# Kernel optimization log

Measured on AMD Instinct MI355X. Metric: run time of the kernel, lower is better.

The kernel has to match this reference:

```python
import jax, jax.numpy as jnp
import numpy as np
import math

B, S, D, H = 2, 2048, 1024, 16
DK = D // H

def setup_inputs() -> dict:
    key = jax.random.key(0)
    ks = jax.random.split(key, 12)
    scale = 0.02
    return {
        "q": jax.random.normal(ks[0], (B, S, D), jnp.float32),
        "k": jax.random.normal(ks[1], (B, S, D), jnp.float32),
        "v": jax.random.normal(ks[2], (B, S, D), jnp.float32),
        "mask": jnp.ones((B, S), jnp.int32),
        "Wq": jax.random.normal(ks[3], (D, D), jnp.float32) * scale,
        "bq": jnp.zeros((D,), jnp.float32),
        "Wk": jax.random.normal(ks[4], (D, D), jnp.float32) * scale,
        "bk": jnp.zeros((D,), jnp.float32),
        "Wv": jax.random.normal(ks[5], (D, D), jnp.float32) * scale,
        "bv": jnp.zeros((D,), jnp.float32),
        "Wo": jax.random.normal(ks[6], (D, D), jnp.float32) * scale,
        "bo": jnp.zeros((D,), jnp.float32),
    }

def _split_heads(x):
    b, s, d = x.shape
    return x.reshape(b, s, H, DK).transpose(0, 2, 1, 3)  # [b,h,s,dk]

def reference(q, k, v, mask, Wq, bq, Wk, bk, Wv, bv, Wo, bo):
    Q = _split_heads(q @ Wq.T + bq)
    K = _split_heads(k @ Wk.T + bk)
    V = _split_heads(v @ Wv.T + bv)
    scores = jnp.einsum('bhqd,bhkd->bhqk', Q, K) / math.sqrt(DK)
    # mask dim==2 path: [b,s] -> [b,1,1,s]
    m = mask[:, None, None, :]
    scores = jnp.where(m == 0, jnp.float32(-1e9), scores)
    attn = jax.nn.softmax(scores, axis=-1)  # dropout is identity in eval
    out = jnp.einsum('bhqk,bhkd->bhqd', attn, V)
    out = out.transpose(0, 2, 1, 3).reshape(q.shape[0], q.shape[1], D)
    return out @ Wo.T + bo
```

## Files before the change

### kernel.cpp

```cpp
#include <hip/hip_runtime.h>
#include <math.h>

#define D_MODEL 1024
#define NHEAD   16
#define DKH     64
#define SEQ     2048
#define BATCH   2
#define TOK     (BATCH*SEQ)

typedef short s16x8 __attribute__((ext_vector_type(8)));
typedef float f32x4 __attribute__((ext_vector_type(4)));
typedef float f32x16 __attribute__((ext_vector_type(16)));
typedef unsigned short ushort_t;

__device__ inline unsigned short f2bf(float f) {
    union { float f; unsigned u; } v; v.f = f;
    unsigned r = v.u + 0x7FFFu + ((v.u >> 16) & 1u);
    return (unsigned short)(r >> 16);
}
__device__ inline float bf2f(ushort_t h) {
    union { unsigned u; float f; } v; v.u = (unsigned)h << 16;
    return v.f;
}
__device__ inline unsigned cvt_pk_bf16(float a, float b) {
    unsigned r;
    asm("v_cvt_pk_bf16_f32 %0, %1, %2" : "=v"(r) : "v"(a), "v"(b));
    return r;
}
__device__ inline void gload16(const void* g, void* l) {
    __builtin_amdgcn_global_load_lds(
        (const __attribute__((address_space(1))) void*)g,
        (__attribute__((address_space(3))) void*)l, 16, 0, 0);
}
__device__ inline f32x16 zero16() {
    f32x16 v;
#pragma unroll
    for (int i = 0; i < 16; ++i) v[i] = 0.f;
    return v;
}

__global__ __launch_bounds__(256) void convert_all(
    const float* __restrict__ q, const float* __restrict__ k,
    const float* __restrict__ v,
    const float* __restrict__ Wq, const float* __restrict__ Wk,
    const float* __restrict__ Wv, const float* __restrict__ Wo,
    const int* __restrict__ mask,
    ushort_t* __restrict__ qb, ushort_t* __restrict__ kb,
    ushort_t* __restrict__ vb,
    ushort_t* __restrict__ Wqb, ushort_t* __restrict__ Wkb,
    ushort_t* __restrict__ Wvb, ushort_t* __restrict__ Wohi,
    ushort_t* __restrict__ Wolo, float* __restrict__ mb)
{
    const int ACT4 = TOK * D_MODEL / 4;
    const int W4   = D_MODEL * D_MODEL / 4;
    const int total = 3 * ACT4 + 4 * W4 + TOK / 4;
    for (int u = blockIdx.x * 256 + threadIdx.x; u < total; u += gridDim.x * 256) {
        if (u < 3 * ACT4) {
            int which = u / ACT4, off = u - which * ACT4;
            const float* src = which == 0 ? q : which == 1 ? k : v;
            ushort_t*    dst = which == 0 ? qb : which == 1 ? kb : vb;
            float4 f = ((const float4*)src)[off];
            uint2 o;
            o.x = cvt_pk_bf16(f.x, f.y);
            o.y = cvt_pk_bf16(f.z, f.w);
            ((uint2*)dst)[off] = o;
        } else if (u < 3 * ACT4 + 3 * W4) {
            int uu = u - 3 * ACT4;
            int which = uu / W4, off = uu - which * W4;
            const float* src = which == 0 ? Wq : which == 1 ? Wk : Wv;
            ushort_t*    dst = which == 0 ? Wqb : which == 1 ? Wkb : Wvb;
            float4 f = ((const float4*)src)[off];
            uint2 o;
            o.x = cvt_pk_bf16(f.x, f.y);
            o.y = cvt_pk_bf16(f.z, f.w);
            ((uint2*)dst)[off] = o;
        } else if (u < 3 * ACT4 + 4 * W4) {
            int off = u - (3 * ACT4 + 3 * W4);
            float4 f = ((const float4*)Wo)[off];
            ushort_t h0 = f2bf(f.x), h1 = f2bf(f.y), h2 = f2bf(f.z), h3 = f2bf(f.w);
            uint2 hw;
            hw.x = (unsigned)h0 | ((unsigned)h1 << 16);
            hw.y = (unsigned)h2 | ((unsigned)h3 << 16);
            ((uint2*)Wohi)[off] = hw;
            uint2 lw;
            lw.x = cvt_pk_bf16(f.x - bf2f(h0), f.y - bf2f(h1));
            lw.y = cvt_pk_bf16(f.z - bf2f(h2), f.w - bf2f(h3));
            ((uint2*)Wolo)[off] = lw;
        } else {
            int off = u - (3 * ACT4 + 4 * W4);
            int4 m = ((const int4*)mask)[off];
            float4 f;
            f.x = m.x ? 0.f : -1e9f;
            f.y = m.y ? 0.f : -1e9f;
            f.z = m.z ? 0.f : -1e9f;
            f.w = m.w ? 0.f : -1e9f;
            ((float4*)mb)[off] = f;
        }
    }
}

__global__ __launch_bounds__(256) void gemm_qkv(
    const ushort_t* __restrict__ qb, const ushort_t* __restrict__ kb,
    const ushort_t* __restrict__ vb,
    const ushort_t* __restrict__ Wqb, const ushort_t* __restrict__ Wkb,
    const ushort_t* __restrict__ Wvb,
    const float* __restrict__ bqp, const float* __restrict__ bkp,
    const float* __restrict__ bvp,
    ushort_t* __restrict__ Qb, ushort_t* __restrict__ Kb,
    ushort_t* __restrict__ Vtb)
{
    __shared__ __align__(16) char pool[64 * 136 * 2];
    ushort_t* As = (ushort_t*)pool;
    ushort_t* Ws = As + 128 * 32;

    const int z = blockIdx.z;
    const ushort_t* Ain  = z == 0 ? qb : z == 1 ? kb : vb;
    const ushort_t* Wptr = z == 0 ? Wqb : z == 1 ? Wkb : Wvb;
    const float*    bias = z == 0 ? bqp : z == 1 ? bkp : bvp;

    const int hwid = blockIdx.x + 8 * blockIdx.y;
    const int work = (hwid & 7) * 32 + (hwid >> 3);
    const int m0 = (work >> 3) * 128;
    const int n0 = (work & 7) * 128;

    const int t = threadIdx.x;
    const int w = t >> 6, lane = t & 63, l15 = lane & 15, l4 = lane >> 4;
    const int wr = w >> 1, wc = w & 1;

    f32x4 acc[4][4];
#pragma unroll
    for (int m = 0; m < 4; ++m)
#pragma unroll
        for (int n = 0; n < 4; ++n) acc[m][n] = (f32x4){0.f, 0.f, 0.f, 0.f};

    const int schunk = (t & 3) ^ ((t >> 2) & 3);
    const ushort_t* Ag = Ain  + (size_t)(m0 + (t >> 2)) * D_MODEL + schunk * 8;
    const ushort_t* Wg = Wptr + (size_t)(n0 + (t >> 2)) * D_MODEL + schunk * 8;
    ushort_t* AsW = As + w * 512;
    ushort_t* WsW = Ws + w * 512;
    const int fx = (l4 ^ (l15 & 3)) * 8;

    for (int k0 = 0; k0 < D_MODEL; k0 += 32) {
        __syncthreads();
        gload16(Ag + k0, AsW);
        gload16(Ag + (size_t)64 * D_MODEL + k0, AsW + 2048);
        gload16(Wg + k0, WsW);
        gload16(Wg + (size_t)64 * D_MODEL + k0, WsW + 2048);
        __syncthreads();

        s16x8 af[4], bfr[4];
#pragma unroll
        for (int m = 0; m < 4; ++m)
            af[m] = *(const s16x8*)&As[(wr * 64 + m * 16 + l15) * 32 + fx];
#pragma unroll
        for (int n = 0; n < 4; ++n)
            bfr[n] = *(const s16x8*)&Ws[(wc * 64 + n * 16 + l15) * 32 + fx];
#pragma unroll
        for (int m = 0; m < 4; ++m)
#pragma unroll
            for (int n = 0; n < 4; ++n)
                acc[m][n] = __builtin_amdgcn_mfma_f32_16x16x32_bf16(af[m], bfr[n], acc[m][n], 0, 0, 0);
    }

    if (z == 2) {
        ushort_t* Ct = (ushort_t*)pool;
        const int h0 = n0 >> 6;
        const int bb = m0 >> 11;
        const int s0 = m0 & (SEQ - 1);
#pragma unroll
        for (int hh = 0; hh < 2; ++hh) {
            __syncthreads();
            if (wc == hh) {
#pragma unroll
                for (int n = 0; n < 4; ++n) {
                    const int nl = n * 16 + l15;
                    const float bv = bias[n0 + hh * 64 + nl];
#pragma unroll
                    for (int m = 0; m < 4; ++m) {
                        const int ml = wr * 64 + m * 16 + l4 * 4;
#pragma unroll
                        for (int r = 0; r < 4; ++r)
                            Ct[nl * 136 + ml + r] = f2bf(acc[m][n][r] + bv);
                    }
                }
            }
            __syncthreads();
            const int dl = t >> 2;
            ushort_t* dst = Vtb + (((size_t)bb * NHEAD + h0 + hh) * DKH + dl) * SEQ + s0;
#pragma unroll
            for (int c = 0; c < 4; ++c) {
                int chk = (t & 3) + c * 4;
                *(uint4*)&dst[chk * 8] = *(const uint4*)&Ct[dl * 136 + chk * 8];
            }
        }
    } else {
        ushort_t* Cout = z == 0 ? Qb : Kb;
#pragma unroll
        for (int n = 0; n < 4; ++n) {
            const int col = n0 + wc * 64 + n * 16 + l15;
            const float bv = bias[col];
#pragma unroll
            for (int m = 0; m < 4; ++m) {
                const int row = m0 + wr * 64 + m * 16 + l4 * 4;
#pragma unroll
                for (int r = 0; r < 4; ++r)
                    Cout[(size_t)(row + r) * D_MODEL + col] = f2bf(acc[m][n][r] + bv);
            }
        }
    }
}

__global__ __launch_bounds__(256) void gemm_out(
    const ushort_t* __restrict__ Ain, const ushort_t* __restrict__ Wptr,
    const ushort_t* __restrict__ W2ptr, const float* __restrict__ bias,
    float* __restrict__ Cout)
{
    __shared__ ushort_t As[128 * 32];
    __shared__ ushort_t Ws[64 * 32];
    __shared__ ushort_t Ws2[64 * 32];

    const int hwid = blockIdx.x + 16 * blockIdx.y;
    const int work = (hwid & 7) * 64 + (hwid >> 3);
    const int m0 = (work >> 4) * 128;
    const int n0 = (work & 15) * 64;

    const int t = threadIdx.x;
    const int w = t >> 6, lane = t & 63, l15 = lane & 15, l4 = lane >> 4;
    const int wr = w >> 1, wc = w & 1;

    f32x4 acc[4][2];
#pragma unroll
    for (int m = 0; m < 4; ++m)
#pragma unroll
        for (int n = 0; n < 2; ++n) acc[m][n] = (f32x4){0.f, 0.f, 0.f, 0.f};

    const int schunk = (t & 3) ^ ((t >> 2) & 3);
    const ushort_t* Ag  = Ain   + (size_t)(m0 + (t >> 2)) * D_MODEL + schunk * 8;
    const ushort_t* Wg  = Wptr  + (size_t)(n0 + (t >> 2)) * D_MODEL + schunk * 8;
    const ushort_t* W2g = W2ptr + (size_t)(n0 + (t >> 2)) * D_MODEL + schunk * 8;
    ushort_t* AsW = As + w * 512;
    ushort_t* WsW = Ws + w * 512;
    ushort_t* Ws2W = Ws2 + w * 512;
    const int fx = (l4 ^ (l15 & 3)) * 8;

    for (int k0 = 0; k0 < D_MODEL; k0 += 32) {
        __syncthreads();
        gload16(Ag + k0, AsW);
        gload16(Ag + (size_t)64 * D_MODEL + k0, AsW + 2048);
        gload16(Wg + k0, WsW);
        gload16(W2g + k0, Ws2W);
        __syncthreads();

        s16x8 af[4], bfr[2], bfr2[2];
#pragma unroll
        for (int m = 0; m < 4; ++m)
            af[m] = *(const s16x8*)&As[(wr * 64 + m * 16 + l15) * 32 + fx];
#pragma unroll
        for (int n = 0; n < 2; ++n) {
            bfr[n]  = *(const s16x8*)&Ws[(wc * 32 + n * 16 + l15) * 32 + fx];
            bfr2[n] = *(const s16x8*)&Ws2[(wc * 32 + n * 16 + l15) * 32 + fx];
        }
#pragma unroll
        for (int m = 0; m < 4; ++m)
#pragma unroll
            for (int n = 0; n < 2; ++n) {
                acc[m][n] = __builtin_amdgcn_mfma_f32_16x16x32_bf16(af[m], bfr[n],  acc[m][n], 0, 0, 0);
                acc[m][n] = __builtin_amdgcn_mfma_f32_16x16x32_bf16(af[m], bfr2[n], acc[m][n], 0, 0, 0);
            }
    }

#pragma unroll
    for (int n = 0; n < 2; ++n) {
        const int col = n0 + wc * 32 + n * 16 + l15;
        const float bv = bias[col];
#pragma unroll
        for (int m = 0; m < 4; ++m) {
            const int row = m0 + wr * 64 + m * 16 + l4 * 4;
#pragma unroll
            for (int r = 0; r < 4; ++r)
                Cout[(size_t)(row + r) * D_MODEL + col] = acc[m][n][r] + bv;
        }
    }
}

__global__ __launch_bounds__(256) void flash5(
    const ushort_t* __restrict__ Q, const ushort_t* __restrict__ K,
    const ushort_t* __restrict__ Vt, const float* __restrict__ mb,
    ushort_t* __restrict__ Ctx)
{
    __shared__ ushort_t Ks[64 * 72];
    __shared__ ushort_t Vs[64 * 72];
    __shared__ ushort_t Ps[128 * 72];

    const int t = threadIdx.x;
    const int w = t >> 6, lane = t & 63;
    const int l31 = lane & 31, lh = lane >> 5;
    const int q0 = blockIdx.y * 128;
    const int bh = blockIdx.x, b = bh >> 4, h = bh & 15;

    s16x8 qf[4];
    {
        const ushort_t* qp = Q + ((size_t)b * SEQ + q0 + w * 32 + l31) * D_MODEL + h * DKH + lh * 8;
#pragma unroll
        for (int ks = 0; ks < 4; ++ks)
            qf[ks] = *(const s16x8*)(qp + ks * 16);
    }

    f32x16 oacc0 = zero16(), oacc1 = zero16();
    float lpart[16];
#pragma unroll
    for (int i = 0; i < 16; ++i) lpart[i] = 0.f;

    const int ch   = t & 7;
    const int row0 = t >> 3;
    const ushort_t* Kg = K  + ((size_t)b * SEQ) * D_MODEL + h * DKH + ch * 8;
    const ushort_t* Vg = Vt + ((size_t)bh * DKH) * SEQ + ch * 8;

    uint4 kr0 = *(const uint4*)&Kg[(size_t)row0 * D_MODEL];
    uint4 kr1 = *(const uint4*)&Kg[(size_t)(row0 + 32) * D_MODEL];
    uint4 vr0 = *(const uint4*)&Vg[(size_t)row0 * SEQ];
    uint4 vr1 = *(const uint4*)&Vg[(size_t)(row0 + 32) * SEQ];

    const float CSC = 0.18033688011112042f;
    const float* mbp = mb + b * SEQ;
    const int prow = w * 32;

    for (int k0 = 0; k0 < SEQ; k0 += 64) {
        __syncthreads();
        *(uint4*)&Ks[row0 * 72 + ch * 8]        = kr0;
        *(uint4*)&Ks[(row0 + 32) * 72 + ch * 8] = kr1;
        *(uint4*)&Vs[row0 * 72 + ch * 8]        = vr0;
        *(uint4*)&Vs[(row0 + 32) * 72 + ch * 8] = vr1;
        __syncthreads();
        if (k0 + 64 < SEQ) {
            kr0 = *(const uint4*)&Kg[(size_t)(k0 + 64 + row0) * D_MODEL];
            kr1 = *(const uint4*)&Kg[(size_t)(k0 + 64 + row0 + 32) * D_MODEL];
            vr0 = *(const uint4*)&Vg[(size_t)row0 * SEQ + k0 + 64];
            vr1 = *(const uint4*)&Vg[(size_t)(row0 + 32) * SEQ + k0 + 64];
        }
        const float mb0 = mbp[k0 + l31];
        const float mb1 = mbp[k0 + 32 + l31];

        f32x16 sacc0 = zero16(), sacc1 = zero16();
        __builtin_amdgcn_s_setprio(1);
#pragma unroll
        for (int ks = 0; ks < 4; ++ks) {
            s16x8 kf0 = *(const s16x8*)&Ks[(l31)      * 72 + ks * 16 + lh * 8];
            s16x8 kf1 = *(const s16x8*)&Ks[(32 + l31) * 72 + ks * 16 + lh * 8];
            sacc0 = __builtin_amdgcn_mfma_f32_32x32x16_bf16(qf[ks], kf0, sacc0, 0, 0, 0);
            sacc1 = __builtin_amdgcn_mfma_f32_32x32x16_bf16(qf[ks], kf1, sacc1, 0, 0, 0);
        }
        __builtin_amdgcn_s_setprio(0);

#pragma unroll
        for (int rp = 0; rp < 8; ++rp) {
            const int r0 = 2 * rp;
            const int rowb = (r0 & 3) + 8 * (r0 >> 2) + 4 * lh;
            float p0 = __builtin_amdgcn_exp2f(fmaf(sacc0[r0],     CSC, mb0));
            float p1 = __builtin_amdgcn_exp2f(fmaf(sacc0[r0 + 1], CSC, mb0));
            float p2 = __builtin_amdgcn_exp2f(fmaf(sacc1[r0],     CSC, mb1));
            float p3 = __builtin_amdgcn_exp2f(fmaf(sacc1[r0 + 1], CSC, mb1));
            lpart[r0]     += p0 + p2;
            lpart[r0 + 1] += p1 + p3;
            unsigned ua = cvt_pk_bf16(p0, p1);
            unsigned ub = cvt_pk_bf16(p2, p3);
            int base0 = (prow + rowb) * 72 + l31;
            Ps[base0]           = (ushort_t)ua;
            Ps[base0 + 72]      = (ushort_t)(ua >> 16);
            Ps[base0 + 32]      = (ushort_t)ub;
            Ps[base0 + 72 + 32] = (ushort_t)(ub >> 16);
        }
        __builtin_amdgcn_sched_barrier(0);

        __builtin_amdgcn_s_setprio(1);
#pragma unroll
        for (int ks = 0; ks < 4; ++ks) {
            s16x8 pa  = *(const s16x8*)&Ps[(prow + l31) * 72 + ks * 16 + lh * 8];
            s16x8 vf0 = *(const s16x8*)&Vs[(l31)      * 72 + ks * 16 + lh * 8];
            s16x8 vf1 = *(const s16x8*)&Vs[(32 + l31) * 72 + ks * 16 + lh * 8];
            oacc0 = __builtin_amdgcn_mfma_f32_32x32x16_bf16(pa, vf0, oacc0, 0, 0, 0);
            oacc1 = __builtin_amdgcn_mfma_f32_32x32x16_bf16(pa, vf1, oacc1, 0, 0, 0);
        }
        __builtin_amdgcn_s_setprio(0);
    }

#pragma unroll
    for (int rg = 0; rg < 16; ++rg) {
        lpart[rg] += __shfl_xor(lpart[rg], 1);
        lpart[rg] += __shfl_xor(lpart[rg], 2);
        lpart[rg] += __shfl_xor(lpart[rg], 4);
        lpart[rg] += __shfl_xor(lpart[rg], 8);
        lpart[rg] += __shfl_xor(lpart[rg], 16);
    }
    const size_t obase = ((size_t)b * SEQ + q0 + w * 32) * D_MODEL + h * DKH + l31;
#pragma unroll
    for (int rg = 0; rg < 16; ++rg) {
        const int qrow = (rg & 3) + 8 * (rg >> 2) + 4 * lh;
        const float inv = 1.f / lpart[rg];
        Ctx[obase + (size_t)qrow * D_MODEL]      = f2bf(oacc0[rg] * inv);
        Ctx[obase + (size_t)qrow * D_MODEL + 32] = f2bf(oacc1[rg] * inv);
    }
}

extern "C" void kernel_launch(void* const* d_in, const int* in_sizes, int n_in,
                              void* d_out, int out_size, void* d_ws, size_t ws_size,
                              hipStream_t stream) {
    const float* q    = (const float*)d_in[0];
    const float* k    = (const float*)d_in[1];
    const float* v    = (const float*)d_in[2];
    const int*   mask = (const int*)  d_in[3];
    const float* Wq   = (const float*)d_in[4];
    const float* bq   = (const float*)d_in[5];
    const float* Wk   = (const float*)d_in[6];
    const float* bk   = (const float*)d_in[7];
    const float* Wv   = (const float*)d_in[8];
    const float* bv   = (const float*)d_in[9];
    const float* Wo   = (const float*)d_in[10];
    const float* bo   = (const float*)d_in[11];
    float* out = (float*)d_out;

    char* ws = (char*)d_ws;
    ushort_t* Wqb  = (ushort_t*)(ws);
    ushort_t* Wkb  = (ushort_t*)(ws + ( 2u << 20));
    ushort_t* Wvb  = (ushort_t*)(ws + ( 4u << 20));
    ushort_t* Wohi = (ushort_t*)(ws + ( 6u << 20));
    ushort_t* Wolo = (ushort_t*)(ws + ( 8u << 20));
    float*    mb   = (float*)   (ws + (10u << 20));
    ushort_t* qb   = (ushort_t*)(ws + (12u << 20));
    ushort_t* kb   = (ushort_t*)(ws + (20u << 20));
    ushort_t* vb   = (ushort_t*)(ws + (28u << 20));
    ushort_t* Qb   = (ushort_t*)(ws + (36u << 20));
    ushort_t* Kb   = (ushort_t*)(ws + (44u << 20));
    ushort_t* Vtb  = (ushort_t*)(ws + (52u << 20));
    ushort_t* Ctx  = qb;

    convert_all<<<2048, 256, 0, stream>>>(q, k, v, Wq, Wk, Wv, Wo, mask,
                                          qb, kb, vb, Wqb, Wkb, Wvb,
                                          Wohi, Wolo, mb);

    dim3 qkvgrid(D_MODEL / 128, TOK / 128, 3);
    gemm_qkv<<<qkvgrid, 256, 0, stream>>>(qb, kb, vb, Wqb, Wkb, Wvb,
                                          bq, bk, bv, Qb, Kb, Vtb);

    dim3 agrid(BATCH * NHEAD, SEQ / 128);
    flash5<<<agrid, 256, 0, stream>>>(Qb, Kb, Vtb, mb, Ctx);

    dim3 ogrid(D_MODEL / 64, TOK / 128);
    gemm_out<<<ogrid, 256, 0, stream>>>(Ctx, Wohi, Wolo, bo, out);
}
```

Baseline: 150.6 us.

## Fuse fp32-to-bf16 activation conversion into QKV GEMM tile loads

Drops the separate pass that converts q/k/v activations to bf16. The QKV GEMM now loads fp32 activation tiles straight into LDS and converts them to bf16 while building MFMA fragments. This removes a full read and write of the three activation tensors, in exchange for twice the LDS footprint and load traffic per A tile. LDS reads of the fp32 tile are no longer swizzled, so bank conflicts are possible.

```diff
diff --git a/kernel.cpp b/kernel.cpp
--- a/kernel.cpp
+++ b/kernel.cpp
@@ -38,35 +38,28 @@
     for (int i = 0; i < 16; ++i) v[i] = 0.f;
     return v;
 }
-
-__global__ __launch_bounds__(256) void convert_all(
-    const float* __restrict__ q, const float* __restrict__ k,
-    const float* __restrict__ v,
+__device__ inline s16x8 cvt8(const float* p) {
+    union { unsigned u[4]; s16x8 v; } r;
+    r.u[0] = cvt_pk_bf16(p[0], p[1]);
+    r.u[1] = cvt_pk_bf16(p[2], p[3]);
+    r.u[2] = cvt_pk_bf16(p[4], p[5]);
+    r.u[3] = cvt_pk_bf16(p[6], p[7]);
+    return r.v;
+}
+
+__global__ __launch_bounds__(256) void convert_w(
     const float* __restrict__ Wq, const float* __restrict__ Wk,
     const float* __restrict__ Wv, const float* __restrict__ Wo,
     const int* __restrict__ mask,
-    ushort_t* __restrict__ qb, ushort_t* __restrict__ kb,
-    ushort_t* __restrict__ vb,
     ushort_t* __restrict__ Wqb, ushort_t* __restrict__ Wkb,
     ushort_t* __restrict__ Wvb, ushort_t* __restrict__ Wohi,
     ushort_t* __restrict__ Wolo, float* __restrict__ mb)
 {
-    const int ACT4 = TOK * D_MODEL / 4;
-    const int W4   = D_MODEL * D_MODEL / 4;
-    const int total = 3 * ACT4 + 4 * W4 + TOK / 4;
+    const int W4 = D_MODEL * D_MODEL / 4;
+    const int total = 4 * W4 + TOK / 4;
     for (int u = blockIdx.x * 256 + threadIdx.x; u < total; u += gridDim.x * 256) {
-        if (u < 3 * ACT4) {
-            int which = u / ACT4, off = u - which * ACT4;
-            const float* src = which == 0 ? q : which == 1 ? k : v;
-            ushort_t*    dst = which == 0 ? qb : which == 1 ? kb : vb;
-            float4 f = ((const float4*)src)[off];
-            uint2 o;
-            o.x = cvt_pk_bf16(f.x, f.y);
-            o.y = cvt_pk_bf16(f.z, f.w);
-            ((uint2*)dst)[off] = o;
-        } else if (u < 3 * ACT4 + 3 * W4) {
-            int uu = u - 3 * ACT4;
-            int which = uu / W4, off = uu - which * W4;
+        if (u < 3 * W4) {
+            int which = u / W4, off = u - which * W4;
             const float* src = which == 0 ? Wq : which == 1 ? Wk : Wv;
             ushort_t*    dst = which == 0 ? Wqb : which == 1 ? Wkb : Wvb;
             float4 f = ((const float4*)src)[off];
@@ -74,8 +67,8 @@
             o.x = cvt_pk_bf16(f.x, f.y);
             o.y = cvt_pk_bf16(f.z, f.w);
             ((uint2*)dst)[off] = o;
-        } else if (u < 3 * ACT4 + 4 * W4) {
-            int off = u - (3 * ACT4 + 3 * W4);
+        } else if (u < 4 * W4) {
+            int off = u - 3 * W4;
             float4 f = ((const float4*)Wo)[off];
             ushort_t h0 = f2bf(f.x), h1 = f2bf(f.y), h2 = f2bf(f.z), h3 = f2bf(f.w);
             uint2 hw;
@@ -87,7 +80,7 @@
             lw.y = cvt_pk_bf16(f.z - bf2f(h2), f.w - bf2f(h3));
             ((uint2*)Wolo)[off] = lw;
         } else {
-            int off = u - (3 * ACT4 + 4 * W4);
+            int off = u - 4 * W4;
             int4 m = ((const int4*)mask)[off];
             float4 f;
             f.x = m.x ? 0.f : -1e9f;
@@ -100,8 +93,8 @@
 }
 
 __global__ __launch_bounds__(256) void gemm_qkv(
-    const ushort_t* __restrict__ qb, const ushort_t* __restrict__ kb,
-    const ushort_t* __restrict__ vb,
+    const float* __restrict__ qin, const float* __restrict__ kin,
+    const float* __restrict__ vin,
     const ushort_t* __restrict__ Wqb, const ushort_t* __restrict__ Wkb,
     const ushort_t* __restrict__ Wvb,
     const float* __restrict__ bqp, const float* __restrict__ bkp,
@@ -109,12 +102,12 @@
     ushort_t* __restrict__ Qb, ushort_t* __restrict__ Kb,
     ushort_t* __restrict__ Vtb)
 {
-    __shared__ __align__(16) char pool[64 * 136 * 2];
-    ushort_t* As = (ushort_t*)pool;
-    ushort_t* Ws = As + 128 * 32;
+    __shared__ __align__(16) char pool[128 * 32 * 4 + 128 * 32 * 2];
+    float*    AsF = (float*)pool;
+    ushort_t* Ws  = (ushort_t*)(pool + 128 * 32 * 4);
 
     const int z = blockIdx.z;
-    const ushort_t* Ain  = z == 0 ? qb : z == 1 ? kb : vb;
+    const float*    Ain  = z == 0 ? qin : z == 1 ? kin : vin;
     const ushort_t* Wptr = z == 0 ? Wqb : z == 1 ? Wkb : Wvb;
     const float*    bias = z == 0 ? bqp : z == 1 ? bkp : bvp;
 
@@ -133,17 +126,21 @@
 #pragma unroll
         for (int n = 0; n < 4; ++n) acc[m][n] = (f32x4){0.f, 0.f, 0.f, 0.f};
 
+    const int arow = w * 8 + (lane >> 3);
+    const int acol = (lane & 7) * 4;
+    const float* Ag = Ain + (size_t)(m0 + arow) * D_MODEL + acol;
+    float* AsW = AsF + w * 256;
+
     const int schunk = (t & 3) ^ ((t >> 2) & 3);
-    const ushort_t* Ag = Ain  + (size_t)(m0 + (t >> 2)) * D_MODEL + schunk * 8;
     const ushort_t* Wg = Wptr + (size_t)(n0 + (t >> 2)) * D_MODEL + schunk * 8;
-    ushort_t* AsW = As + w * 512;
     ushort_t* WsW = Ws + w * 512;
     const int fx = (l4 ^ (l15 & 3)) * 8;
 
     for (int k0 = 0; k0 < D_MODEL; k0 += 32) {
         __syncthreads();
-        gload16(Ag + k0, AsW);
-        gload16(Ag + (size_t)64 * D_MODEL + k0, AsW + 2048);
+#pragma unroll
+        for (int i = 0; i < 4; ++i)
+            gload16(Ag + (size_t)(i * 32) * D_MODEL + k0, AsW + i * 1024);
         gload16(Wg + k0, WsW);
         gload16(Wg + (size_t)64 * D_MODEL + k0, WsW + 2048);
         __syncthreads();
@@ -151,7 +148,7 @@
         s16x8 af[4], bfr[4];
 #pragma unroll
         for (int m = 0; m < 4; ++m)
-            af[m] = *(const s16x8*)&As[(wr * 64 + m * 16 + l15) * 32 + fx];
+            af[m] = cvt8(&AsF[(wr * 64 + m * 16 + l15) * 32 + l4 * 8]);
 #pragma unroll
         for (int n = 0; n < 4; ++n)
             bfr[n] = *(const s16x8*)&Ws[(wc * 64 + n * 16 + l15) * 32 + fx];
@@ -426,20 +423,16 @@
     ushort_t* Wohi = (ushort_t*)(ws + ( 6u << 20));
     ushort_t* Wolo = (ushort_t*)(ws + ( 8u << 20));
     float*    mb   = (float*)   (ws + (10u << 20));
-    ushort_t* qb   = (ushort_t*)(ws + (12u << 20));
-    ushort_t* kb   = (ushort_t*)(ws + (20u << 20));
-    ushort_t* vb   = (ushort_t*)(ws + (28u << 20));
-    ushort_t* Qb   = (ushort_t*)(ws + (36u << 20));
-    ushort_t* Kb   = (ushort_t*)(ws + (44u << 20));
-    ushort_t* Vtb  = (ushort_t*)(ws + (52u << 20));
-    ushort_t* Ctx  = qb;
-
-    convert_all<<<2048, 256, 0, stream>>>(q, k, v, Wq, Wk, Wv, Wo, mask,
-                                          qb, kb, vb, Wqb, Wkb, Wvb,
-                                          Wohi, Wolo, mb);
+    ushort_t* Ctx  = (ushort_t*)(ws + (12u << 20));
+    ushort_t* Qb   = (ushort_t*)(ws + (20u << 20));
+    ushort_t* Kb   = (ushort_t*)(ws + (28u << 20));
+    ushort_t* Vtb  = (ushort_t*)(ws + (36u << 20));
+
+    convert_w<<<1024, 256, 0, stream>>>(Wq, Wk, Wv, Wo, mask,
+                                        Wqb, Wkb, Wvb, Wohi, Wolo, mb);
 
     dim3 qkvgrid(D_MODEL / 128, TOK / 128, 3);
-    gemm_qkv<<<qkvgrid, 256, 0, stream>>>(qb, kb, vb, Wqb, Wkb, Wvb,
+    gemm_qkv<<<qkvgrid, 256, 0, stream>>>(q, k, v, Wqb, Wkb, Wvb,
                                           bq, bk, bv, Qb, Kb, Vtb);
 
     dim3 agrid(BATCH * NHEAD, SEQ / 128);
```

New measurement: 293.5 us. +94.9%, slower.
